# Optimization experiments

Measured on AMD Instinct MI355X. Metric: run time of the kernel, lower is better.

Reference implementation:

```python
import jax, jax.numpy as jnp
import numpy as np

B, T, D_MODEL, H, D = 2, 2048, 1024, 16, 64
EPS = 1e-5


def _layernorm(x, g, b):
    m = jnp.mean(x, axis=-1, keepdims=True)
    v = jnp.var(x, axis=-1, keepdims=True)
    return (x - m) * jax.lax.rsqrt(v + EPS) * g + b


def setup_inputs() -> dict:
    key = jax.random.key(0)
    ks = jax.random.split(key, 5)
    qab = H * D
    x = jax.random.normal(ks[0], (B, T, D_MODEL), dtype=jnp.float32)
    sc = 1.0 / np.sqrt(D_MODEL)
    Wq = jax.random.normal(ks[1], (D_MODEL, qab), dtype=jnp.float32) * sc
    Wa = jax.random.normal(ks[2], (D_MODEL, qab), dtype=jnp.float32) * sc
    Wb = jax.random.normal(ks[3], (D_MODEL, qab), dtype=jnp.float32) * sc
    Wo = jax.random.normal(ks[4], (qab, D_MODEL), dtype=jnp.float32) * (1.0 / np.sqrt(qab))
    g = jnp.ones((D,), dtype=jnp.float32)
    z = jnp.zeros((D,), dtype=jnp.float32)
    return {"x": x, "Wq": Wq, "Wa": Wa, "Wb": Wb, "Wo": Wo,
            "q_gamma": g, "q_beta": z, "a_gamma": g, "a_beta": z,
            "b_gamma": g, "b_beta": z}


def reference(x, Wq, Wa, Wb, Wo, q_gamma, q_beta, a_gamma, a_beta, b_gamma, b_beta):
    def split_heads(y):  # (B,T,H*D) -> (B,H,T,D)
        Bx, Tx, _ = y.shape
        return y.reshape(Bx, Tx, H, D).transpose(0, 2, 1, 3)

    q = _layernorm(split_heads(x @ Wq), q_gamma, q_beta)
    a = _layernorm(split_heads(x @ Wa), a_gamma, a_beta)
    b = _layernorm(split_heads(x @ Wb), b_gamma, b_beta)

    # strict-exclusive cumsum of a along time
    a_excl = jnp.cumsum(a, axis=-2) - a
    # o_t = q_t . sum_{j<=t} a_excl_j (x) b_j  ==  causal (q a_excl^T) b
    scores = jnp.einsum('bhtd,bhsd->bhts', q, a_excl)  # (B,H,T,T)
    causal = jnp.tril(jnp.ones((T, T), dtype=scores.dtype))  # j <= t
    o = jnp.einsum('bhts,bhse->bhte', scores * causal, b)  # (B,H,T,D)

    o = o.transpose(0, 2, 1, 3).reshape(B, T, H * D)  # merge heads
    return o @ Wo
```

## Files before the change

kernel.cpp:

```cpp
#include <hip/hip_runtime.h>
#include <hip/hip_bf16.h>

#define T_LEN  2048
#define NHEAD  16
#define HDIM   64
#define DMODEL 1024
#define BATCH  2
#define MROWS  4096
#define L_CHK  64
#define N_CHK  (T_LEN / L_CHK)
#define BH     (BATCH * NHEAD)
#define LSTR   72

typedef __attribute__((ext_vector_type(8))) short short8;
typedef __attribute__((ext_vector_type(4))) float f32x4;
typedef __attribute__((ext_vector_type(4))) unsigned short ushort4v;

#define GLDS(GP, LP) __builtin_amdgcn_global_load_lds( \
    (__attribute__((address_space(1))) void*)(void*)(GP), \
    (__attribute__((address_space(3))) void*)(LP), 16, 0, 0)

__device__ __forceinline__ unsigned short f2bf(float f) {
  union { float f; unsigned int u; } v; v.f = f;
  unsigned int r = v.u + 0x7FFFu + ((v.u >> 16) & 1u);
  return (unsigned short)(r >> 16);
}
__device__ __forceinline__ float bf2f(short s) {
  union { unsigned int u; float f; } v;
  v.u = ((unsigned int)(unsigned short)s) << 16;
  return v.f;
}

__global__ __launch_bounds__(256) void ha_conv(
    const float* __restrict__ Wq, const float* __restrict__ Wa,
    const float* __restrict__ Wb, const float* __restrict__ Wo,
    const float* __restrict__ X,
    short* __restrict__ wqabT, short* __restrict__ woT,
    short* __restrict__ Xb) {
  const int z = blockIdx.z;
  const int tid = threadIdx.x;
  if (z == 4) {
    const int bidl = blockIdx.y * 16 + blockIdx.x;
    #pragma unroll
    for (int p = 0; p < 8; ++p) {
      const size_t idx = (size_t)bidl * 16384 + (size_t)p * 2048 + tid * 8;
      float4 v0 = *(const float4*)(X + idx);
      float4 v1 = *(const float4*)(X + idx + 4);
      short8 o;
      o[0] = (short)f2bf(v0.x); o[1] = (short)f2bf(v0.y);
      o[2] = (short)f2bf(v0.z); o[3] = (short)f2bf(v0.w);
      o[4] = (short)f2bf(v1.x); o[5] = (short)f2bf(v1.y);
      o[6] = (short)f2bf(v1.z); o[7] = (short)f2bf(v1.w);
      *(short8*)(Xb + idx) = o;
    }
    return;
  }
  __shared__ float tile[64][65];
  const float* W = (z == 0) ? Wq : (z == 1) ? Wa : (z == 2) ? Wb : Wo;
  short* WT = (z < 3) ? wqabT + (size_t)z * 1024 * DMODEL : woT;
  const int k0 = blockIdx.y * 64, n0 = blockIdx.x * 64;
  #pragma unroll
  for (int p = 0; p < 4; ++p) {
    const int r  = p * 16 + (tid >> 4);
    const int c4 = (tid & 15) * 4;
    float4 v = *(const float4*)(W + (size_t)(k0 + r) * DMODEL + n0 + c4);
    tile[r][c4 + 0] = v.x; tile[r][c4 + 1] = v.y;
    tile[r][c4 + 2] = v.z; tile[r][c4 + 3] = v.w;
  }
  __syncthreads();
  #pragma unroll
  for (int p = 0; p < 4; ++p) {
    const int n = p * 16 + (tid >> 4);
    const int c = (tid & 15) * 4;
    ushort4v o = { f2bf(tile[c + 0][n]), f2bf(tile[c + 1][n]),
                   f2bf(tile[c + 2][n]), f2bf(tile[c + 3][n]) };
    *(ushort4v*)(WT + (size_t)(n0 + n) * DMODEL + k0 + c) = o;
  }
}

__global__ __launch_bounds__(256) void ha_gemm_qab(
    const short* __restrict__ Ab, const short* __restrict__ Bt,
    short* __restrict__ q, short* __restrict__ a, short* __restrict__ bOut,
    const float* __restrict__ qg, const float* __restrict__ qbet,
    const float* __restrict__ ag, const float* __restrict__ abet,
    const float* __restrict__ bg, const float* __restrict__ bbet) {
  __shared__ short As[128 * 32] __attribute__((aligned(16)));
  __shared__ short Bs[128 * 32] __attribute__((aligned(16)));
  const int tid = threadIdx.x;
  const int wave = tid >> 6, lane = tid & 63;
  const int m0  = blockIdx.y * 128;
  const int n0g = blockIdx.x * 128;
  short* Cbuf; const float* gamma; const float* beta;
  if (n0g < 1024)      { Cbuf = q;    gamma = qg; beta = qbet; }
  else if (n0g < 2048) { Cbuf = a;    gamma = ag; beta = abet; }
  else                 { Cbuf = bOut; gamma = bg; beta = bbet; }
  const int n0 = n0g & 1023;

  const int srow = wave * 32 + (lane >> 2);
  const int scol = (lane & 3) * 8;
  const short* agp = Ab + (size_t)(m0 + srow) * DMODEL + scol;
  const short* bgp = Bt + (size_t)(n0g + srow) * DMODEL + scol;
  short* alp = As + wave * 32 * 32;
  short* blp = Bs + wave * 32 * 32;

  f32x4 acc[4][4] = {};
  const int lm = lane & 15, kh = lane >> 4;
  const int wm = (wave >> 1) * 64, wn = (wave & 1) * 64;

  float gl[4], bl[4];
  #pragma unroll
  for (int j = 0; j < 4; ++j) {
    gl[j] = gamma[j * 16 + lm];
    bl[j] = beta[j * 16 + lm];
  }

  for (int k0 = 0; k0 < DMODEL; k0 += 32) {
    GLDS(agp,               alp);
    GLDS(agp + 16 * DMODEL, alp + 16 * 32);
    GLDS(bgp,               blp);
    GLDS(bgp + 16 * DMODEL, blp + 16 * 32);
    agp += 32; bgp += 32;
    __syncthreads();
    short8 af[4], bf[4];
    #pragma unroll
    for (int i = 0; i < 4; ++i) {
      af[i] = *(const short8*)&As[(wm + i * 16 + lm) * 32 + kh * 8];
      bf[i] = *(const short8*)&Bs[(wn + i * 16 + lm) * 32 + kh * 8];
    }
    #pragma unroll
    for (int i = 0; i < 4; ++i)
      #pragma unroll
      for (int j = 0; j < 4; ++j)
        acc[i][j] = __builtin_amdgcn_mfma_f32_16x16x32_bf16(
            af[i], bf[j], acc[i][j], 0, 0, 0);
    __syncthreads();
  }

  #pragma unroll
  for (int i = 0; i < 4; ++i) {
    float s1[4] = {0.f, 0.f, 0.f, 0.f};
    float s2[4] = {0.f, 0.f, 0.f, 0.f};
    #pragma unroll
    for (int j = 0; j < 4; ++j)
      #pragma unroll
      for (int r = 0; r < 4; ++r) {
        const float v = acc[i][j][r];
        s1[r] += v; s2[r] += v * v;
      }
    #pragma unroll
    for (int m = 1; m <= 8; m <<= 1)
      #pragma unroll
      for (int r = 0; r < 4; ++r) {
        s1[r] += __shfl_xor(s1[r], m);
        s2[r] += __shfl_xor(s2[r], m);
      }
    #pragma unroll
    for (int r = 0; r < 4; ++r) {
      const float mean = s1[r] * 0.015625f;
      const float var  = s2[r] * 0.015625f - mean * mean;
      const float rs   = rsqrtf(var + 1e-5f);
      short* cp = Cbuf + (size_t)(m0 + wm + i * 16 + kh * 4 + r) * DMODEL +
                  n0 + wn + lm;
      #pragma unroll
      for (int j = 0; j < 4; ++j)
        cp[j * 16] = (short)f2bf((acc[i][j][r] - mean) * rs * gl[j] + bl[j]);
    }
  }
}

__global__ __launch_bounds__(256) void ha_gemm_out(
    const short* __restrict__ Ab, const short* __restrict__ Bt,
    float* __restrict__ C) {
  __shared__ short As[128 * 32] __attribute__((aligned(16)));
  __shared__ short Bs[64 * 32] __attribute__((aligned(16)));
  const int tid = threadIdx.x;
  const int wave = tid >> 6, lane = tid & 63;
  const int m0 = blockIdx.y * 128;
  const int n0 = blockIdx.x * 64;

  const int arow = wave * 32 + (lane >> 2);
  const int brow = wave * 16 + (lane >> 2);
  const int scol = (lane & 3) * 8;
  const short* agp = Ab + (size_t)(m0 + arow) * DMODEL + scol;
  const short* bgp = Bt + (size_t)(n0 + brow) * DMODEL + scol;
  short* alp = As + wave * 32 * 32;
  short* blp = Bs + wave * 16 * 32;

  f32x4 acc[4][2] = {};
  const int lm = lane & 15, kh = lane >> 4;
  const int wm = (wave >> 1) * 64, wn = (wave & 1) * 32;

  for (int k0 = 0; k0 < DMODEL; k0 += 32) {
    GLDS(agp,               alp);
    GLDS(agp + 16 * DMODEL, alp + 16 * 32);
    GLDS(bgp,               blp);
    agp += 32; bgp += 32;
    __syncthreads();
    short8 af[4], bf2[2];
    #pragma unroll
    for (int i = 0; i < 4; ++i)
      af[i] = *(const short8*)&As[(wm + i * 16 + lm) * 32 + kh * 8];
    #pragma unroll
    for (int j = 0; j < 2; ++j)
      bf2[j] = *(const short8*)&Bs[(wn + j * 16 + lm) * 32 + kh * 8];
    #pragma unroll
    for (int i = 0; i < 4; ++i)
      #pragma unroll
      for (int j = 0; j < 2; ++j)
        acc[i][j] = __builtin_amdgcn_mfma_f32_16x16x32_bf16(
            af[i], bf2[j], acc[i][j], 0, 0, 0);
    __syncthreads();
  }
  #pragma unroll
  for (int i = 0; i < 4; ++i)
    #pragma unroll
    for (int j = 0; j < 2; ++j) {
      float* cp = C + (size_t)(m0 + wm + i * 16 + kh * 4) * DMODEL +
                  n0 + wn + j * 16 + lm;
      #pragma unroll
      for (int r = 0; r < 4; ++r) cp[(size_t)r * DMODEL] = acc[i][j][r];
    }
}

__global__ __launch_bounds__(256) void ha_scan1(
    const short* __restrict__ An, const short* __restrict__ Bn,
    float* __restrict__ M, float* __restrict__ Asums, float* __restrict__ Bsums) {
  __shared__ short Btl[64 * LSTR] __attribute__((aligned(16)));
  __shared__ short Ltl[64 * LSTR] __attribute__((aligned(16)));
  __shared__ float sega[4][64];
  __shared__ float segb[4][64];
  const int bid = blockIdx.x;
  const int c   = bid & (N_CHK - 1);
  const int bh  = bid >> 5;
  const int b = bh >> 4, h = bh & 15;
  const int tid = threadIdx.x;
  const size_t rowbase = ((size_t)b * T_LEN + (size_t)c * L_CHK) * DMODEL + h * HDIM;
  const size_t vec = ((size_t)bh * N_CHK + c) * 64;

  #pragma unroll
  for (int i = 0; i < 2; ++i) {
    const int idx = tid + 256 * i;
    const int s = idx >> 3, c8 = (idx & 7) * 8;
    short8 b8 = *(const short8*)(Bn + rowbase + (size_t)s * DMODEL + c8);
    #pragma unroll
    for (int k = 0; k < 8; ++k) Btl[(c8 + k) * LSTR + s] = b8[k];
  }

  const int d = tid & 63, seg = tid >> 6;
  {
    float run = 0.f;
    for (int s = seg * 16; s < seg * 16 + 16; ++s) {
      const float v = bf2f(An[rowbase + (size_t)s * DMODEL + d]);
      Ltl[d * LSTR + s] = (short)f2bf(run);
      run += v;
    }
    sega[seg][d] = run;
  }
  __syncthreads();
  {
    float off = 0.f;
    for (int qq = 0; qq < seg; ++qq) off += sega[qq][d];
    #pragma unroll
    for (int g = 0; g < 2; ++g) {
      short8 v = *(short8*)&Ltl[d * LSTR + seg * 16 + g * 8];
      #pragma unroll
      for (int k = 0; k < 8; ++k) v[k] = (short)f2bf(bf2f(v[k]) + off);
      *(short8*)&Ltl[d * LSTR + seg * 16 + g * 8] = v;
    }
    if (seg == 3) Asums[vec + d] = off + sega[3][d];
    float sb = 0.f;
    #pragma unroll
    for (int g = 0; g < 2; ++g) {
      short8 v = *(const short8*)&Btl[d * LSTR + seg * 16 + g * 8];
      #pragma unroll
      for (int k = 0; k < 8; ++k) sb += bf2f(v[k]);
    }
    segb[seg][d] = sb;
  }
  __syncthreads();
  if (tid < 64)
    Bsums[vec + tid] = segb[0][tid] + segb[1][tid] + segb[2][tid] + segb[3][tid];

  const int wave = tid >> 6, lane = tid & 63;
  const int lm = lane & 15, quad = lane >> 4;
  const int estrip = wave * 16;
  f32x4 acc[4] = {};
  #pragma unroll
  for (int kk = 0; kk < 2; ++kk) {
    short8 afr = *(const short8*)&Btl[(estrip + lm) * LSTR + kk * 32 + quad * 8];
    #pragma unroll
    for (int j = 0; j < 4; ++j) {
      short8 bfr = *(const short8*)&Ltl[(j * 16 + lm) * LSTR + kk * 32 + quad * 8];
      acc[j] = __builtin_amdgcn_mfma_f32_16x16x32_bf16(afr, bfr, acc[j], 0, 0, 0);
    }
  }
  float* Mp = M + vec * 64;
  #pragma unroll
  for (int j = 0; j < 4; ++j)
    #pragma unroll
    for (int r = 0; r < 4; ++r)
      Mp[(estrip + quad * 4 + r) * 64 + j * 16 + lm] = acc[j][r];
}

__global__ __launch_bounds__(256) void ha_s2p(
    const float* __restrict__ M, const float* __restrict__ Asums,
    const float* __restrict__ Bsums, float* __restrict__ Aoff,
    short* __restrict__ Soffb) {
  __shared__ float ao[N_CHK][64];
  const int part = blockIdx.x & 7;
  const int bh   = blockIdx.x >> 3;
  const int tid  = threadIdx.x;
  for (int i = tid; i < N_CHK * 64; i += 256)
    ao[i >> 6][i & 63] = Asums[(size_t)bh * N_CHK * 64 + i];
  __syncthreads();
  if (tid < 64) {
    float run = 0.f;
    for (int c = 0; c < N_CHK; ++c) {
      const float v = ao[c][tid];
      ao[c][tid] = run;
      run += v;
    }
  }
  __syncthreads();
  if (part == 0)
    for (int i = tid; i < N_CHK * 64; i += 256)
      Aoff[(size_t)bh * N_CHK * 64 + i] = ao[i >> 6][i & 63];

  const int e = part * 8 + (tid >> 5);
  const int d = (tid & 31) * 2;
  float2 S = make_float2(0.f, 0.f);
  const float* Mp = M + (size_t)bh * N_CHK * 4096 + e * 64 + d;
  const float* Bp = Bsums + (size_t)bh * N_CHK * 64 + e;
  short* Sp = Soffb + (size_t)bh * N_CHK * 4096 + e * 64 + d;
  float2 m = *(const float2*)Mp;
  float bs = *Bp;
  for (int c = 0; c < N_CHK; ++c) {
    const int cn = (c + 1 < N_CHK) ? c + 1 : c;
    const float2 mn = *(const float2*)(Mp + (size_t)cn * 4096);
    const float bsn = Bp[(size_t)cn * 64];
    const unsigned pk = (unsigned)f2bf(S.x) | ((unsigned)f2bf(S.y) << 16);
    *(unsigned*)(Sp + (size_t)c * 4096) = pk;
    S.x += fmaf(bs, ao[c][d], m.x);
    S.y += fmaf(bs, ao[c][d + 1], m.y);
    m = mn; bs = bsn;
  }
}

__global__ __launch_bounds__(256) void ha_scan3(
    const short* __restrict__ Qn, const short* __restrict__ An,
    const short* __restrict__ Bn, const short* __restrict__ Soffb,
    const float* __restrict__ Aoff, short* __restrict__ Ob) {
  __shared__ short Qs [64 * LSTR] __attribute__((aligned(16)));
  __shared__ short Gs [64 * LSTR] __attribute__((aligned(16)));
  __shared__ short Btl[64 * LSTR] __attribute__((aligned(16)));
  __shared__ short Ssl[64 * LSTR] __attribute__((aligned(16)));
  __shared__ short Ptl[64 * LSTR] __attribute__((aligned(16)));
  __shared__ float sega[4][64];
  const int bid = blockIdx.x;
  const int c   = bid & (N_CHK - 1);
  const int bh  = bid >> 5;
  const int b = bh >> 4, h = bh & 15;
  const int tid = threadIdx.x;
  const size_t rowbase = ((size_t)b * T_LEN + (size_t)c * L_CHK) * DMODEL + h * HDIM;
  const size_t vec = ((size_t)bh * N_CHK + c) * 64;

  #pragma unroll
  for (int i = 0; i < 2; ++i) {
    const int idx = tid + 256 * i;
    const int r = idx >> 3, c8 = (idx & 7) * 8;
    short8 q8 = *(const short8*)(Qn + rowbase + (size_t)r * DMODEL + c8);
    *(short8*)&Qs[r * LSTR + c8] = q8;
    short8 s8 = *(const short8*)(Soffb + vec * 64 + (size_t)r * 64 + c8);
    *(short8*)&Ssl[r * LSTR + c8] = s8;
    short8 b8 = *(const short8*)(Bn + rowbase + (size_t)r * DMODEL + c8);
    #pragma unroll
    for (int k = 0; k < 8; ++k) Btl[(c8 + k) * LSTR + r] = b8[k];
  }

  const int d = tid & 63, seg = tid >> 6;
  {
    float run = 0.f;
    for (int s = seg * 16; s < seg * 16 + 16; ++s) {
      const float v = bf2f(An[rowbase + (size_t)s * DMODEL + d]);
      Gs[s * LSTR + d] = (short)f2bf(run);
      run += v;
    }
    sega[seg][d] = run;
  }
  __syncthreads();
  {
    float off = Aoff[vec + d];
    for (int qq = 0; qq < seg; ++qq) off += sega[qq][d];
    for (int s = seg * 16; s < seg * 16 + 16; ++s)
      Gs[s * LSTR + d] = (short)f2bf(bf2f(Gs[s * LSTR + d]) + off);
  }
  __syncthreads();

  const int wave = tid >> 6, lane = tid & 63;
  const int lm = lane & 15, quad = lane >> 4;
  const int tstrip = wave * 16;
  {
    f32x4 p[4] = {};
    #pragma unroll
    for (int kk = 0; kk < 2; ++kk) {
      short8 qf = *(const short8*)&Qs[(tstrip + lm) * LSTR + kk * 32 + quad * 8];
      #pragma unroll
      for (int j = 0; j < 4; ++j) {
        short8 gf = *(const short8*)&Gs[(j * 16 + lm) * LSTR + kk * 32 + quad * 8];
        p[j] = __builtin_amdgcn_mfma_f32_16x16x32_bf16(qf, gf, p[j], 0, 0, 0);
      }
    }
    #pragma unroll
    for (int j = 0; j < 4; ++j)
      #pragma unroll
      for (int r = 0; r < 4; ++r) {
        const int t = tstrip + quad * 4 + r;
        const int s = j * 16 + lm;
        Ptl[t * LSTR + s] = (s <= t) ? (short)f2bf(p[j][r]) : (short)0;
      }
  }
  __syncthreads();

  {
    f32x4 o[4] = {};
    #pragma unroll
    for (int kk = 0; kk < 2; ++kk) {
      short8 pf = *(const short8*)&Ptl[(tstrip + lm) * LSTR + kk * 32 + quad * 8];
      #pragma unroll
      for (int j = 0; j < 4; ++j) {
        short8 bfr = *(const short8*)&Btl[(j * 16 + lm) * LSTR + kk * 32 + quad * 8];
        o[j] = __builtin_amdgcn_mfma_f32_16x16x32_bf16(pf, bfr, o[j], 0, 0, 0);
      }
    }
    #pragma unroll
    for (int kk = 0; kk < 2; ++kk) {
      short8 qf = *(const short8*)&Qs[(tstrip + lm) * LSTR + kk * 32 + quad * 8];
      #pragma unroll
      for (int j = 0; j < 4; ++j) {
        short8 sf = *(const short8*)&Ssl[(j * 16 + lm) * LSTR + kk * 32 + quad * 8];
        o[j] = __builtin_amdgcn_mfma_f32_16x16x32_bf16(qf, sf, o[j], 0, 0, 0);
      }
    }
    #pragma unroll
    for (int j = 0; j < 4; ++j)
      #pragma unroll
      for (int r = 0; r < 4; ++r) {
        const int t = tstrip + quad * 4 + r;
        const int e = j * 16 + lm;
        Ob[rowbase + (size_t)t * DMODEL + e] = (short)f2bf(o[j][r]);
      }
  }
}

extern "C" void kernel_launch(void* const* d_in, const int* in_sizes, int n_in,
                              void* d_out, int out_size, void* d_ws,
                              size_t ws_size, hipStream_t stream) {
  const float* x  = (const float*)d_in[0];
  const float* Wq = (const float*)d_in[1];
  const float* Wa = (const float*)d_in[2];
  const float* Wb = (const float*)d_in[3];
  const float* Wo = (const float*)d_in[4];
  const float* qg = (const float*)d_in[5];
  const float* qb = (const float*)d_in[6];
  const float* ag = (const float*)d_in[7];
  const float* ab = (const float*)d_in[8];
  const float* bg = (const float*)d_in[9];
  const float* bb = (const float*)d_in[10];
  float* out = (float*)d_out;

  char* ws = (char*)d_ws;
  short* qn  = (short*)(ws);
  short* an  = (short*)(ws + ((size_t)8  << 20));
  short* bn  = (short*)(ws + ((size_t)16 << 20));
  short* xb  = (short*)(ws + ((size_t)24 << 20));
  short* obb = xb;
  short* wqabT = (short*)(ws + ((size_t)32 << 20));
  short* woT   = (short*)(ws + ((size_t)38 << 20));
  float* asums = (float*)(ws + ((size_t)40 << 20));
  float* bsums = asums + (size_t)BH * N_CHK * 64;
  float* aoff  = bsums + (size_t)BH * N_CHK * 64;
  short* soffb = (short*)(ws + ((size_t)42 << 20));
  float* Mbuf  = out;

  ha_conv<<<dim3(16, 16, 5), 256, 0, stream>>>(Wq, Wa, Wb, Wo, x,
                                               wqabT, woT, xb);

  ha_gemm_qab<<<dim3(24, 32), 256, 0, stream>>>(xb, wqabT, qn, an, bn,
                                                qg, qb, ag, ab, bg, bb);

  ha_scan1<<<BH * N_CHK, 256, 0, stream>>>(an, bn, Mbuf, asums, bsums);
  ha_s2p<<<BH * 8, 256, 0, stream>>>(Mbuf, asums, bsums, aoff, soffb);
  ha_scan3<<<BH * N_CHK, 256, 0, stream>>>(qn, an, bn, soffb, aoff, obb);

  ha_gemm_out<<<dim3(16, 32), 256, 0, stream>>>(obb, woT, out);
}
```

Before: 182.3 us.

## Stage epilogue stores through LDS and store chunk state matrices in bf16

The QAB GEMM epilogue and the scan3 output now stage bf16 results in shared memory and write them out as coalesced 16-byte vector stores, replacing scattered 2-byte stores. The per-chunk state matrix M passed from scan1 to s2p is stored as bf16 instead of fp32, halving that intermediate traffic. s2p also prefetches two chunks ahead. Costs are extra LDS, added barriers, and reduced precision in the carried chunk-state sums.

New measurement: 200.0 us. 9.7% more time.

```diff
diff --git a/kernel.cpp b/kernel.cpp
--- a/kernel.cpp
+++ b/kernel.cpp
@@ -86,6 +86,7 @@
     const float* __restrict__ bg, const float* __restrict__ bbet) {
   __shared__ short As[128 * 32] __attribute__((aligned(16)));
   __shared__ short Bs[128 * 32] __attribute__((aligned(16)));
+  __shared__ short Stg[64 * 136] __attribute__((aligned(16)));
   const int tid = threadIdx.x;
   const int wave = tid >> 6, lane = tid & 63;
   const int m0  = blockIdx.y * 128;
@@ -159,12 +160,39 @@
       const float mean = s1[r] * 0.015625f;
       const float var  = s2[r] * 0.015625f - mean * mean;
       const float rs   = rsqrtf(var + 1e-5f);
-      short* cp = Cbuf + (size_t)(m0 + wm + i * 16 + kh * 4 + r) * DMODEL +
-                  n0 + wn + lm;
       #pragma unroll
       for (int j = 0; j < 4; ++j)
-        cp[j * 16] = (short)f2bf((acc[i][j][r] - mean) * rs * gl[j] + bl[j]);
-    }
+        acc[i][j][r] = (acc[i][j][r] - mean) * rs * gl[j] + bl[j];
+    }
+  }
+
+  #pragma unroll
+  for (int pass = 0; pass < 2; ++pass) {
+    if (wm == pass * 64) {
+      #pragma unroll
+      for (int i = 0; i < 4; ++i)
+        #pragma unroll
+        for (int r = 0; r < 4; ++r)
+          #pragma unroll
+          for (int j = 0; j < 4; ++j)
+            Stg[(i * 16 + kh * 4 + r) * 136 + wn + j * 16 + lm] =
+                (short)f2bf(acc[i][j][r]);
+    }
+    __syncthreads();
+    {
+      const int row = tid >> 2, seg = tid & 3;
+      const short* sp = &Stg[row * 136 + seg * 32];
+      short8 v0 = *(const short8*)(sp);
+      short8 v1 = *(const short8*)(sp + 8);
+      short8 v2 = *(const short8*)(sp + 16);
+      short8 v3 = *(const short8*)(sp + 24);
+      short* cp = Cbuf + (size_t)(m0 + pass * 64 + row) * DMODEL + n0 + seg * 32;
+      *(short8*)cp        = v0;
+      *(short8*)(cp + 8)  = v1;
+      *(short8*)(cp + 16) = v2;
+      *(short8*)(cp + 24) = v3;
+    }
+    __syncthreads();
   }
 }
 
@@ -224,7 +252,7 @@
 
 __global__ __launch_bounds__(256) void ha_scan1(
     const short* __restrict__ An, const short* __restrict__ Bn,
-    float* __restrict__ M, float* __restrict__ Asums, float* __restrict__ Bsums) {
+    short* __restrict__ M, float* __restrict__ Asums, float* __restrict__ Bsums) {
   __shared__ short Btl[64 * LSTR] __attribute__((aligned(16)));
   __shared__ short Ltl[64 * LSTR] __attribute__((aligned(16)));
   __shared__ float sega[4][64];
@@ -294,16 +322,16 @@
       acc[j] = __builtin_amdgcn_mfma_f32_16x16x32_bf16(afr, bfr, acc[j], 0, 0, 0);
     }
   }
-  float* Mp = M + vec * 64;
+  short* Mp = M + vec * 64;
   #pragma unroll
   for (int j = 0; j < 4; ++j)
     #pragma unroll
     for (int r = 0; r < 4; ++r)
-      Mp[(estrip + quad * 4 + r) * 64 + j * 16 + lm] = acc[j][r];
+      Mp[(estrip + quad * 4 + r) * 64 + j * 16 + lm] = (short)f2bf(acc[j][r]);
 }
 
 __global__ __launch_bounds__(256) void ha_s2p(
-    const float* __restrict__ M, const float* __restrict__ Asums,
+    const short* __restrict__ M, const float* __restrict__ Asums,
     const float* __restrict__ Bsums, float* __restrict__ Aoff,
     short* __restrict__ Soffb) {
   __shared__ float ao[N_CHK][64];
@@ -329,20 +357,21 @@
   const int e = part * 8 + (tid >> 5);
   const int d = (tid & 31) * 2;
   float2 S = make_float2(0.f, 0.f);
-  const float* Mp = M + (size_t)bh * N_CHK * 4096 + e * 64 + d;
+  const short* Mp = M + (size_t)bh * N_CHK * 4096 + e * 64 + d;
   const float* Bp = Bsums + (size_t)bh * N_CHK * 64 + e;
   short* Sp = Soffb + (size_t)bh * N_CHK * 4096 + e * 64 + d;
-  float2 m = *(const float2*)Mp;
-  float bs = *Bp;
+  unsigned mr0 = *(const unsigned*)Mp;
+  unsigned mr1 = *(const unsigned*)(Mp + 4096);
+  float bs0 = Bp[0], bs1 = Bp[64];
   for (int c = 0; c < N_CHK; ++c) {
-    const int cn = (c + 1 < N_CHK) ? c + 1 : c;
-    const float2 mn = *(const float2*)(Mp + (size_t)cn * 4096);
-    const float bsn = Bp[(size_t)cn * 64];
+    const int c2 = (c + 2 < N_CHK) ? c + 2 : c;
+    const unsigned mrn = *(const unsigned*)(Mp + (size_t)c2 * 4096);
+    const float bsn = Bp[(size_t)c2 * 64];
     const unsigned pk = (unsigned)f2bf(S.x) | ((unsigned)f2bf(S.y) << 16);
     *(unsigned*)(Sp + (size_t)c * 4096) = pk;
-    S.x += fmaf(bs, ao[c][d], m.x);
-    S.y += fmaf(bs, ao[c][d + 1], m.y);
-    m = mn; bs = bsn;
+    S.x += fmaf(bs0, ao[c][d],     bf2f((short)(mr0 & 0xffffu)));
+    S.y += fmaf(bs0, ao[c][d + 1], bf2f((short)(mr0 >> 16)));
+    mr0 = mr1; mr1 = mrn; bs0 = bs1; bs1 = bsn;
   }
 }
 
@@ -444,11 +473,17 @@
     #pragma unroll
     for (int j = 0; j < 4; ++j)
       #pragma unroll
-      for (int r = 0; r < 4; ++r) {
-        const int t = tstrip + quad * 4 + r;
-        const int e = j * 16 + lm;
-        Ob[rowbase + (size_t)t * DMODEL + e] = (short)f2bf(o[j][r]);
-      }
+      for (int r = 0; r < 4; ++r)
+        Gs[(tstrip + quad * 4 + r) * LSTR + j * 16 + lm] = (short)f2bf(o[j][r]);
+  }
+  __syncthreads();
+  {
+    const int t = tid >> 2, seg2 = tid & 3;
+    short8 v0 = *(const short8*)&Gs[t * LSTR + seg2 * 16];
+    short8 v1 = *(const short8*)&Gs[t * LSTR + seg2 * 16 + 8];
+    short* op = Ob + rowbase + (size_t)t * DMODEL + seg2 * 16;
+    *(short8*)op       = v0;
+    *(short8*)(op + 8) = v1;
   }
 }
 
@@ -480,7 +515,7 @@
   float* bsums = asums + (size_t)BH * N_CHK * 64;
   float* aoff  = bsums + (size_t)BH * N_CHK * 64;
   short* soffb = (short*)(ws + ((size_t)42 << 20));
-  float* Mbuf  = out;
+  short* Mbuf  = (short*)out;
 
   ha_conv<<<dim3(16, 16, 5), 256, 0, stream>>>(Wq, Wa, Wb, Wo, x,
                                                wqabT, woT, xb);
```
